# Kernel tuning notes

Measured on AMD Instinct MI355X. Metric: run time of the kernel, lower is better.

Reference implementation:

```python
import jax, jax.numpy as jnp
import numpy as np

N_NODES = 100000
N_EDGES = 3200000
D_IN = 128
D_OUT = 128


def setup_inputs() -> dict:
    key = jax.random.key(0)
    k1, k2, k3, k4, k5, k6 = jax.random.split(key, 6)
    x = jax.random.normal(k1, (N_NODES, D_IN), dtype=jnp.float32)
    stdv = 1.0 / np.sqrt(D_OUT)
    weight = jax.random.normal(k2, (D_IN, D_OUT), dtype=jnp.float32) * stdv
    bias = jax.random.normal(k3, (D_OUT,), dtype=jnp.float32) * stdv
    edge_row = jax.random.randint(k4, (N_EDGES,), 0, N_NODES, dtype=jnp.int32)
    edge_col = jax.random.randint(k5, (N_EDGES,), 0, N_NODES, dtype=jnp.int32)
    edge_vals = jax.random.uniform(k6, (N_EDGES,), dtype=jnp.float32)
    return {"x": x, "weight": weight, "bias": bias,
            "edge_row": edge_row, "edge_col": edge_col, "edge_vals": edge_vals}


def reference(x, weight, bias, edge_row, edge_col, edge_vals):
    # support = input @ W   (dense GEMM, [N, D_out])
    support = x @ weight
    # spmm = adj @ support  with adj in COO form: out[r] += v * support[c]
    messages = edge_vals[:, None] * support[edge_col]  # [E, D_out]
    agg = jax.ops.segment_sum(messages, edge_row, num_segments=N_NODES)
    return agg + bias
```

## Files before the change

kernel.cpp:

```cpp
#include <hip/hip_runtime.h>

#define D 128
#define NBK_MAX 800
#define T_TILES 256
#define LBUF 4608
#define SLOT_STRIDE 8192

__device__ __forceinline__ unsigned bf16_rne(float f) {
    const unsigned u = __float_as_uint(f);
    return (u + 0x7FFFu + ((u >> 16) & 1u)) >> 16;
}
__device__ __forceinline__ float bf_lo(unsigned u) { return __uint_as_float(u << 16); }
__device__ __forceinline__ float bf_hi(unsigned u) { return __uint_as_float(u & 0xFFFF0000u); }

__global__ __launch_bounds__(256, 2) void gcn_gemm(const float* __restrict__ x,
                                                   const float* __restrict__ w,
                                                   unsigned* __restrict__ support,
                                                   int n_nodes) {
    __shared__ float xs[128][32];
    __shared__ float ws[32][128];
    const int t = threadIdx.x;
    const int rg = t >> 4;
    const int cg = t & 15;
    const long row_base = (long)blockIdx.x * 128;

    float4 acc[8][2];
#pragma unroll
    for (int j = 0; j < 8; ++j) {
        acc[j][0] = make_float4(0.f, 0.f, 0.f, 0.f);
        acc[j][1] = make_float4(0.f, 0.f, 0.f, 0.f);
    }

    for (int s = 0; s < 4; ++s) {
        const int k0 = s * 32;
        {
            const float4* w4 = (const float4*)(w + (long)k0 * D);
            float4* wl = (float4*)&ws[0][0];
#pragma unroll
            for (int i = 0; i < 4; ++i) wl[t + 256 * i] = w4[t + 256 * i];
        }
        {
#pragma unroll
            for (int i = 0; i < 4; ++i) {
                const int f = t + 256 * i;
                const int r = f >> 3;
                const int jj = f & 7;
                long gr = row_base + r;
                if (gr >= n_nodes) gr = n_nodes - 1;
                const float4 v = ((const float4*)(x + gr * D + k0))[jj];
                const int cs = (jj * 4 + 8 * (r >> 3)) & 31;
                ((float4*)&xs[r][0])[cs >> 2] = v;
            }
        }
        __syncthreads();

        const int xrot = 8 * rg;
#pragma unroll 1
        for (int kk = 0; kk < 32; kk += 4) {
            float4 wq[4][2];
#pragma unroll
            for (int d = 0; d < 4; ++d) {
                const float4* wr = (const float4*)&ws[kk + d][0];
                wq[d][0] = wr[cg];
                wq[d][1] = wr[cg + 16];
            }
            const int xi = ((kk + xrot) & 31) >> 2;
#pragma unroll
            for (int j = 0; j < 8; ++j) {
                const float4 xv = ((const float4*)&xs[rg * 8 + j][0])[xi];
#define FMA4(A, S, W) A.x += S * W.x; A.y += S * W.y; A.z += S * W.z; A.w += S * W.w
                FMA4(acc[j][0], xv.x, wq[0][0]); FMA4(acc[j][1], xv.x, wq[0][1]);
                FMA4(acc[j][0], xv.y, wq[1][0]); FMA4(acc[j][1], xv.y, wq[1][1]);
                FMA4(acc[j][0], xv.z, wq[2][0]); FMA4(acc[j][1], xv.z, wq[2][1]);
                FMA4(acc[j][0], xv.w, wq[3][0]); FMA4(acc[j][1], xv.w, wq[3][1]);
#undef FMA4
            }
        }
        __syncthreads();
    }

#pragma unroll
    for (int j = 0; j < 8; ++j) {
        const long r = row_base + rg * 8 + j;
        if (r < n_nodes) {
            uint2 p0, p1;
            p0.x = bf16_rne(acc[j][0].x) | (bf16_rne(acc[j][0].y) << 16);
            p0.y = bf16_rne(acc[j][0].z) | (bf16_rne(acc[j][0].w) << 16);
            p1.x = bf16_rne(acc[j][1].x) | (bf16_rne(acc[j][1].y) << 16);
            p1.y = bf16_rne(acc[j][1].z) | (bf16_rne(acc[j][1].w) << 16);
            ((uint2*)support)[r * 32 + cg] = p0;
            ((uint2*)support)[r * 32 + 16 + cg] = p1;
        }
    }
}

__global__ __launch_bounds__(1024) void gcn_binpass(const int* __restrict__ erow,
                                                    const int* __restrict__ ecol,
                                                    const float* __restrict__ eval,
                                                    int* __restrict__ cursor,
                                                    int2* __restrict__ slots,
                                                    int n_edges, int tile_sz, int nb,
                                                    int n64) {
    __shared__ int h[NBK_MAX];
    const int t = threadIdx.x;
    for (int i = t; i < nb; i += 1024) h[i] = 0;
    __syncthreads();
    const int beg = blockIdx.x * tile_sz;
    const int end = min(beg + tile_sz, n_edges);
    for (int e = beg + t; e < end; e += 1024)
        atomicAdd(&h[erow[e] >> 7], 1);
    __syncthreads();
    for (int i = t; i < nb; i += 1024) {
        const int c = h[i];
        if (c) h[i] = atomicAdd(&cursor[i], c);
    }
    __syncthreads();
    for (int e = beg + t; e < end; e += 1024) {
        const int r = erow[e];
        const int b = r >> 7;
        const int rel = atomicAdd(&h[b], 1);
        const int cap = min(SLOT_STRIDE, n64 - b * SLOT_STRIDE);
        if (rel < cap) {
            const unsigned key = ((unsigned)(r & 127) << 17) | (unsigned)ecol[e];
            slots[(long)b * SLOT_STRIDE + rel] = make_int2((int)key, __float_as_int(eval[e]));
        }
    }
}

__global__ __launch_bounds__(512) void gcn_sort_agg(const uint4* __restrict__ support4,
                                                    const int2* __restrict__ slots,
                                                    const int* __restrict__ cnt,
                                                    const float* __restrict__ bias,
                                                    float* __restrict__ out,
                                                    int n_nodes, int block_base) {
    __shared__ int2 eds[LBUF];
    __shared__ int lrp[129];
    __shared__ int cur[128];
    __shared__ int hist[128];
    __shared__ int scan[128];

    const int t = threadIdx.x;
    const int cb = blockIdx.x + block_base;
    const int cap = min(SLOT_STRIDE, n_nodes * 64 - cb * SLOT_STRIDE);
    const int n = min(min(cnt[cb], cap), LBUF);
    const int2* src = slots + (long)cb * SLOT_STRIDE;

    if (t < 128) hist[t] = 0;
    __syncthreads();
    for (int i = t; i < n; i += 512)
        atomicAdd(&hist[(unsigned)src[i].x >> 17], 1);
    __syncthreads();
    if (t < 128) scan[t] = hist[t];
    __syncthreads();
#pragma unroll
    for (int off = 1; off < 128; off <<= 1) {
        int v = 0;
        if (t < 128 && t >= off) v = scan[t - off];
        __syncthreads();
        if (t < 128) scan[t] += v;
        __syncthreads();
    }
    if (t < 128) {
        const int excl = scan[t] - hist[t];
        lrp[t] = excl;
        cur[t] = excl;
        if (t == 127) lrp[128] = scan[127];
    }
    __syncthreads();
    for (int i = t; i < n; i += 512) {
        const int2 ed = src[i];
        const int rl = (int)((unsigned)ed.x >> 17);
        const int pos = atomicAdd(&cur[rl], 1);
        eds[pos] = make_int2(ed.x & 0x1FFFF, ed.y);
    }
    __syncthreads();

    const int lane = t & 63;
    const int w = t >> 6;
    const int sub = lane & 15;
    const int g = lane >> 4;

    for (int j = 0; j < 16; ++j) {
        const int rl = w * 16 + j;
        const long gr = (long)cb * 128 + rl;
        if (gr >= n_nodes) break;
        const int s0 = lrp[rl];
        const int s1 = lrp[rl + 1];

        float acc[8];
#pragma unroll
        for (int k = 0; k < 8; ++k) acc[k] = 0.f;

#pragma unroll 2
        for (int i = s0 + g; i < s1; i += 4) {
            const int2 ed = eds[i];
            const float v = __int_as_float(ed.y);
            const uint4 pv = support4[(long)ed.x * 16 + sub];
            acc[0] += v * bf_lo(pv.x);
            acc[1] += v * bf_hi(pv.x);
            acc[2] += v * bf_lo(pv.y);
            acc[3] += v * bf_hi(pv.y);
            acc[4] += v * bf_lo(pv.z);
            acc[5] += v * bf_hi(pv.z);
            acc[6] += v * bf_lo(pv.w);
            acc[7] += v * bf_hi(pv.w);
        }

#pragma unroll
        for (int k = 0; k < 8; ++k) {
            acc[k] += __shfl_xor(acc[k], 16, 64);
            acc[k] += __shfl_xor(acc[k], 32, 64);
        }

        if (g == 0) {
            const float4 b0 = ((const float4*)bias)[sub * 2];
            const float4 b1 = ((const float4*)bias)[sub * 2 + 1];
            float4 o0 = make_float4(acc[0] + b0.x, acc[1] + b0.y,
                                    acc[2] + b0.z, acc[3] + b0.w);
            float4 o1 = make_float4(acc[4] + b1.x, acc[5] + b1.y,
                                    acc[6] + b1.z, acc[7] + b1.w);
            float4* orow = (float4*)(out + gr * D);
            orow[sub * 2] = o0;
            orow[sub * 2 + 1] = o1;
        }
    }
}

extern "C" void kernel_launch(void* const* d_in, const int* in_sizes, int n_in,
                              void* d_out, int out_size, void* d_ws, size_t ws_size,
                              hipStream_t stream) {
    const float* x    = (const float*)d_in[0];
    const float* w    = (const float*)d_in[1];
    const float* bias = (const float*)d_in[2];
    const int* erow   = (const int*)d_in[3];
    const int* ecol   = (const int*)d_in[4];
    const float* eval = (const float*)d_in[5];

    const int n_nodes = in_sizes[0] / D;
    const int n_edges = in_sizes[3];
    const int nb = (n_nodes + 127) >> 7;
    const int tile_sz = (n_edges + T_TILES - 1) / T_TILES;

    char* ws = (char*)d_ws;
    unsigned* support = (unsigned*)ws;
    size_t off = (size_t)n_nodes * (D / 2) * sizeof(unsigned);
    int* cursor = (int*)(ws + off);

    int2* slots = (int2*)d_out;
    float* out = (float*)d_out;

    gcn_gemm<<<(n_nodes + 127) / 128, 256, 0, stream>>>(x, w, support, n_nodes);

    hipMemsetAsync(cursor, 0, (size_t)nb * sizeof(int), stream);
    gcn_binpass<<<T_TILES, 1024, 0, stream>>>(erow, ecol, eval, cursor, slots,
                                              n_edges, tile_sz, nb, n_nodes * 64);

    const int nb1 = (nb * 2) / 3;
    gcn_sort_agg<<<nb1, 512, 0, stream>>>((const uint4*)support, slots, cursor,
                                          bias, out, n_nodes, 0);
    gcn_sort_agg<<<nb - nb1, 512, 0, stream>>>((const uint4*)support, slots, cursor,
                                               bias, out, n_nodes, nb1);
}
```

Before: 367.7 us.

## Fuse GEMM and edge binning into one launch; merge split aggregation launches

The dense GEMM and the edge-binning pass are merged into one kernel. The first 256 blocks do binning with 256 threads each, reusing the GEMM shared-memory buffer as the histogram, and the remaining blocks compute the GEMM tiles, so the two independent phases can overlap on the GPU. The two split sort/aggregate launches are also collapsed into one. The tradeoffs are fewer threads per binning block, which means longer per-block edge loops, and possible load imbalance between the two block types.

```diff
diff --git a/kernel.cpp b/kernel.cpp
--- a/kernel.cpp
+++ b/kernel.cpp
@@ -2,7 +2,7 @@
 
 #define D 128
 #define NBK_MAX 800
-#define T_TILES 256
+#define T_BIN 256
 #define LBUF 4608
 #define SLOT_STRIDE 8192
 
@@ -13,16 +13,53 @@
 __device__ __forceinline__ float bf_lo(unsigned u) { return __uint_as_float(u << 16); }
 __device__ __forceinline__ float bf_hi(unsigned u) { return __uint_as_float(u & 0xFFFF0000u); }
 
-__global__ __launch_bounds__(256, 2) void gcn_gemm(const float* __restrict__ x,
-                                                   const float* __restrict__ w,
-                                                   unsigned* __restrict__ support,
-                                                   int n_nodes) {
+__global__ __launch_bounds__(256, 2) void gcn_gemm_bin(const float* __restrict__ x,
+                                                       const float* __restrict__ w,
+                                                       unsigned* __restrict__ support,
+                                                       const int* __restrict__ erow,
+                                                       const int* __restrict__ ecol,
+                                                       const float* __restrict__ eval,
+                                                       int* __restrict__ cursor,
+                                                       int2* __restrict__ slots,
+                                                       int n_nodes, int n_edges,
+                                                       int nb, int nbin) {
     __shared__ float xs[128][32];
     __shared__ float ws[32][128];
     const int t = threadIdx.x;
+
+    if ((int)blockIdx.x < nbin) {
+        int* h = (int*)&xs[0][0];
+        for (int i = t; i < nb; i += 256) h[i] = 0;
+        __syncthreads();
+        const int tile_sz = (n_edges + nbin - 1) / nbin;
+        const int beg = blockIdx.x * tile_sz;
+        const int end = min(beg + tile_sz, n_edges);
+        for (int e = beg + t; e < end; e += 256)
+            atomicAdd(&h[erow[e] >> 7], 1);
+        __syncthreads();
+        for (int i = t; i < nb; i += 256) {
+            const int c = h[i];
+            if (c) h[i] = atomicAdd(&cursor[i], c);
+        }
+        __syncthreads();
+        const int n64 = n_nodes * 64;
+        for (int e = beg + t; e < end; e += 256) {
+            const int r = erow[e];
+            const int b = r >> 7;
+            const int rel = atomicAdd(&h[b], 1);
+            const int cap = min(SLOT_STRIDE, n64 - b * SLOT_STRIDE);
+            if (rel < cap) {
+                const unsigned key = ((unsigned)(r & 127) << 17) | (unsigned)ecol[e];
+                slots[(long)b * SLOT_STRIDE + rel] =
+                    make_int2((int)key, __float_as_int(eval[e]));
+            }
+        }
+        return;
+    }
+
     const int rg = t >> 4;
     const int cg = t & 15;
-    const long row_base = (long)blockIdx.x * 128;
+    const long row_base = (long)(blockIdx.x - nbin) * 128;
 
     float4 acc[8][2];
 #pragma unroll
@@ -94,45 +131,12 @@
     }
 }
 
-__global__ __launch_bounds__(1024) void gcn_binpass(const int* __restrict__ erow,
-                                                    const int* __restrict__ ecol,
-                                                    const float* __restrict__ eval,
-                                                    int* __restrict__ cursor,
-                                                    int2* __restrict__ slots,
-                                                    int n_edges, int tile_sz, int nb,
-                                                    int n64) {
-    __shared__ int h[NBK_MAX];
-    const int t = threadIdx.x;
-    for (int i = t; i < nb; i += 1024) h[i] = 0;
-    __syncthreads();
-    const int beg = blockIdx.x * tile_sz;
-    const int end = min(beg + tile_sz, n_edges);
-    for (int e = beg + t; e < end; e += 1024)
-        atomicAdd(&h[erow[e] >> 7], 1);
-    __syncthreads();
-    for (int i = t; i < nb; i += 1024) {
-        const int c = h[i];
-        if (c) h[i] = atomicAdd(&cursor[i], c);
-    }
-    __syncthreads();
-    for (int e = beg + t; e < end; e += 1024) {
-        const int r = erow[e];
-        const int b = r >> 7;
-        const int rel = atomicAdd(&h[b], 1);
-        const int cap = min(SLOT_STRIDE, n64 - b * SLOT_STRIDE);
-        if (rel < cap) {
-            const unsigned key = ((unsigned)(r & 127) << 17) | (unsigned)ecol[e];
-            slots[(long)b * SLOT_STRIDE + rel] = make_int2((int)key, __float_as_int(eval[e]));
-        }
-    }
-}
-
 __global__ __launch_bounds__(512) void gcn_sort_agg(const uint4* __restrict__ support4,
                                                     const int2* __restrict__ slots,
                                                     const int* __restrict__ cnt,
                                                     const float* __restrict__ bias,
                                                     float* __restrict__ out,
-                                                    int n_nodes, int block_base) {
+                                                    int n_nodes) {
     __shared__ int2 eds[LBUF];
     __shared__ int lrp[129];
     __shared__ int cur[128];
@@ -140,7 +144,7 @@
     __shared__ int scan[128];
 
     const int t = threadIdx.x;
-    const int cb = blockIdx.x + block_base;
+    const int cb = blockIdx.x;
     const int cap = min(SLOT_STRIDE, n_nodes * 64 - cb * SLOT_STRIDE);
     const int n = min(min(cnt[cb], cap), LBUF);
     const int2* src = slots + (long)cb * SLOT_STRIDE;
@@ -239,7 +243,7 @@
     const int n_nodes = in_sizes[0] / D;
     const int n_edges = in_sizes[3];
     const int nb = (n_nodes + 127) >> 7;
-    const int tile_sz = (n_edges + T_TILES - 1) / T_TILES;
+    const int ntile = (n_nodes + 127) >> 7;
 
     char* ws = (char*)d_ws;
     unsigned* support = (unsigned*)ws;
@@ -249,15 +253,11 @@
     int2* slots = (int2*)d_out;
     float* out = (float*)d_out;
 
-    gcn_gemm<<<(n_nodes + 127) / 128, 256, 0, stream>>>(x, w, support, n_nodes);
-
     hipMemsetAsync(cursor, 0, (size_t)nb * sizeof(int), stream);
-    gcn_binpass<<<T_TILES, 1024, 0, stream>>>(erow, ecol, eval, cursor, slots,
-                                              n_edges, tile_sz, nb, n_nodes * 64);
-
-    const int nb1 = (nb * 2) / 3;
-    gcn_sort_agg<<<nb1, 512, 0, stream>>>((const uint4*)support, slots, cursor,
-                                          bias, out, n_nodes, 0);
-    gcn_sort_agg<<<nb - nb1, 512, 0, stream>>>((const uint4*)support, slots, cursor,
-                                               bias, out, n_nodes, nb1);
-}
+    gcn_gemm_bin<<<T_BIN + ntile, 256, 0, stream>>>(
+        x, w, support, erow, ecol, eval, cursor, slots,
+        n_nodes, n_edges, nb, T_BIN);
+
+    gcn_sort_agg<<<nb, 512, 0, stream>>>((const uint4*)support, slots, cursor,
+                                         bias, out, n_nodes);
+}
```

After: 345.0 us. 1.07x faster.
